# Performance work log

Hardware: AMD Instinct MI355X
Metric: run time of the kernel (lower is better)

Reference implementation:

```python
import jax, jax.numpy as jnp
import numpy as np

EPS = 1e-12

def _l2norm(x):
    # F.normalize(p=2, dim=1)
    n = jnp.sqrt(jnp.sum(x * x, axis=1, keepdims=True))
    return x / jnp.maximum(n, EPS)

def _sage(h, c, W, b):
    # Bundler: Linear(concat(h, mean_neigh)) -> l2 normalize -> relu
    z = jnp.concatenate([h, c], axis=1) @ W + b
    return jax.nn.relu(_l2norm(z))

def _block_diag(blocks):
    # blocks: [B, K, K] -> dense [B*K, B*K] block-diagonal (torch.block_diag of per-graph S^T A S)
    B, K, _ = blocks.shape
    out = jnp.zeros((B * K, B * K), blocks.dtype)
    base = (jnp.arange(B) * K)[:, None, None]
    r = base + jnp.arange(K)[None, :, None]
    c = base + jnp.arange(K)[None, None, :]
    return out.at[r, c].set(blocks)

def setup_inputs() -> dict:
    key = jax.random.key(0)
    k0, k1, k2, k3, k4 = jax.random.split(key, 5)
    B, n, F, K, E = 64, 1024, 128, 128, 16384
    N = B * n
    h = jax.random.normal(k0, (N, F), dtype=jnp.float32)
    src_local = jax.random.randint(k1, (B, E), 0, n, dtype=jnp.int32)
    dst_local = jax.random.randint(k2, (B, E), 0, n, dtype=jnp.int32)
    s = 1.0 / np.sqrt(2 * F)
    W_feat = jax.random.normal(k3, (2 * F, F), dtype=jnp.float32) * s
    b_feat = jnp.zeros((F,), dtype=jnp.float32)
    W_pool = jax.random.normal(k4, (2 * F, K), dtype=jnp.float32) * s
    b_pool = jnp.zeros((K,), dtype=jnp.float32)
    return {"h": h, "src_local": src_local, "dst_local": dst_local,
            "W_feat": W_feat, "b_feat": b_feat, "W_pool": W_pool, "b_pool": b_pool}

def reference(h, src_local, dst_local, W_feat, b_feat, W_pool, b_pool):
    N, F = h.shape
    B, E = src_local.shape
    n = N // B
    K = W_pool.shape[1]
    # per-graph local edge ids -> global ids (batched graph)
    off = (jnp.arange(B, dtype=src_local.dtype) * n)[:, None]
    src = (src_local + off).reshape(-1)  # [B*E]
    dst = (dst_local + off).reshape(-1)
    # MeanAggregator: c[i] = mean over in-neighbors (edges src->dst) of h[src]
    deg = jax.ops.segment_sum(jnp.ones((B * E,), h.dtype), dst, num_segments=N)
    c = jax.ops.segment_sum(h[src], dst, num_segments=N) / jnp.maximum(deg, 1.0)[:, None]
    feat = _sage(h, c, W_feat, b_feat)                     # [N, F]
    assign = jax.nn.softmax(_sage(h, c, W_pool, b_pool), axis=1)  # [N, K] per-graph soft assignment
    # adj_external(transpose=True): adj[u, v] = 1 for edge (u -> v)
    # AS[u] = sum over edges (u->v) of assign[v]
    AS = jax.ops.segment_sum(assign[dst], src, num_segments=N)    # [N, K]
    S_r = assign.reshape(B, n, K)
    AS_r = AS.reshape(B, n, K)
    feat_r = feat.reshape(B, n, F)
    # h_new = S^T feat (block-diagonal S => per-graph contraction)
    h_new = jnp.einsum('bnk,bnf->bkf', S_r, feat_r).reshape(B * K, F)
    # adj_new = S^T (adj S), block diagonal across graphs
    blocks = jnp.einsum('bnk,bnl->bkl', S_r, AS_r)
    adj_new = _block_diag(blocks)
    return adj_new, h_new
```

## Files before the change

### kernel.cpp

```cpp
#include <hip/hip_runtime.h>
#include <hip/hip_bf16.h>
#include <cstddef>

#define B_    64
#define NPG   1024
#define F_    128
#define K_    128
#define E_    16384
#define N_    (B_*NPG)
#define BE_   (B_*E_)
#define ADJ_DIM 8192
#define ADJ_ELEMS 67108864UL

typedef __bf16 bf16x8 __attribute__((ext_vector_type(8)));
typedef float  f32x4  __attribute__((ext_vector_type(4)));

__device__ inline float b2f(unsigned short u) {
  return __uint_as_float(((unsigned)u) << 16);
}
__device__ inline unsigned short f2b(float f) {
  __bf16 b = (__bf16)f;
  return *reinterpret_cast<unsigned short*>(&b);
}

__global__ void k_hbf(const float* __restrict__ h, unsigned short* __restrict__ hb) {
  int i = blockIdx.x * 256 + threadIdx.x;
  float4 v = reinterpret_cast<const float4*>(h)[i];
  ushort4 o;
  o.x = f2b(v.x); o.y = f2b(v.y); o.z = f2b(v.z); o.w = f2b(v.w);
  reinterpret_cast<ushort4*>(hb)[i] = o;
}

__global__ void k_count(const int* __restrict__ srcl, const int* __restrict__ dstl,
                        int* __restrict__ deg_in, int* __restrict__ deg_out) {
  int i = blockIdx.x * 256 + threadIdx.x;
  int b = i >> 14;
  int base = b << 10;
  atomicAdd(&deg_in[dstl[i] + base], 1);
  atomicAdd(&deg_out[srcl[i] + base], 1);
}

__global__ __launch_bounds__(1024) void k_scan(const int* __restrict__ deg,
                                               int* __restrict__ off, int* __restrict__ cur) {
  int b = blockIdx.x, t = threadIdx.x;
  int v = deg[b * NPG + t];
  int lane = t & 63, wid = t >> 6;
  int x = v;
  #pragma unroll
  for (int d = 1; d < 64; d <<= 1) {
    int y = __shfl_up(x, d, 64);
    if (lane >= d) x += y;
  }
  __shared__ int wsum[16];
  if (lane == 63) wsum[wid] = x;
  __syncthreads();
  if (t < 16) {
    int s = wsum[t];
    #pragma unroll
    for (int d = 1; d < 16; d <<= 1) {
      int y = __shfl_up(s, d, 16);
      if (t >= d) s += y;
    }
    wsum[t] = s;
  }
  __syncthreads();
  int woff = wid ? wsum[wid - 1] : 0;
  int o = b * E_ + woff + x - v;
  off[b * NPG + t] = o;
  cur[b * NPG + t] = o;
}

__global__ void k_build(const int* __restrict__ srcl, const int* __restrict__ dstl,
                        int* __restrict__ cur_in, int* __restrict__ cur_out,
                        int* __restrict__ ebd_src, int* __restrict__ ebs_dst) {
  int i = blockIdx.x * 256 + threadIdx.x;
  int b = i >> 14;
  int base = b << 10;
  int s = srcl[i] + base, d = dstl[i] + base;
  int p = atomicAdd(&cur_in[d], 1);
  ebd_src[p] = s;
  int q = atomicAdd(&cur_out[s], 1);
  ebs_dst[q] = d;
}

__global__ void k_gather_c(const unsigned short* __restrict__ hb, const int* __restrict__ elist,
                           const int* __restrict__ off, const int* __restrict__ deg,
                           unsigned short* __restrict__ cb, float* __restrict__ adj) {
  {
    float4 z4 = make_float4(0.f, 0.f, 0.f, 0.f);
    float4* dst = reinterpret_cast<float4*>(adj) + (size_t)blockIdx.x * 1024 + threadIdx.x;
    #pragma unroll
    for (int r = 0; r < 4; ++r) dst[r * 256] = z4;
  }
  int w = threadIdx.x >> 6, lane = threadIdx.x & 63;
  int node = blockIdx.x * 4 + w;
  int o = off[node], d = deg[node];
  float accx = 0.f, accy = 0.f;
  int e = o, end = o + d;
  while (e < end) {
    int cnt = end - e; if (cnt > 64) cnt = 64;
    int sidx = (lane < cnt) ? elist[e + lane] : 0;
    for (int j = 0; j < cnt; ++j) {
      int s = __shfl(sidx, j, 64);
      unsigned v = *reinterpret_cast<const unsigned*>(hb + (size_t)s * 128 + lane * 2);
      accx += __uint_as_float((v & 0xffffu) << 16);
      accy += __uint_as_float(v & 0xffff0000u);
    }
    e += cnt;
  }
  float inv = 1.0f / fmaxf((float)d, 1.0f);
  accx *= inv; accy *= inv;
  unsigned ov = (unsigned)f2b(accx) | ((unsigned)f2b(accy) << 16);
  *reinterpret_cast<unsigned*>(cb + (size_t)node * 128 + lane * 2) = ov;
}

__global__ void k_gather_as(const unsigned short* __restrict__ rows, const int* __restrict__ elist,
                            const int* __restrict__ off, const int* __restrict__ deg,
                            unsigned short* __restrict__ outb) {
  int w = threadIdx.x >> 6, lane = threadIdx.x & 63;
  int node = blockIdx.x * 4 + w;
  int o = off[node], d = deg[node];
  float accx = 0.f, accy = 0.f;
  int e = o, end = o + d;
  while (e < end) {
    int cnt = end - e; if (cnt > 64) cnt = 64;
    int sidx = (lane < cnt) ? elist[e + lane] : 0;
    for (int j = 0; j < cnt; ++j) {
      int s = __shfl(sidx, j, 64);
      unsigned v = *reinterpret_cast<const unsigned*>(rows + (size_t)s * 256 + lane * 2);
      accx += __uint_as_float((v & 0xffffu) << 16);
      accy += __uint_as_float(v & 0xffff0000u);
    }
    e += cnt;
  }
  unsigned ov = (unsigned)f2b(accx) | ((unsigned)f2b(accy) << 16);
  *reinterpret_cast<unsigned*>(outb + (size_t)node * 128 + lane * 2) = ov;
}

__global__ void k_wt(const float* __restrict__ Wf, const float* __restrict__ Wp,
                     __bf16* __restrict__ Wt) {
  int j = blockIdx.x;
  int k = threadIdx.x;
  const float* W = (j < 128) ? Wf : Wp;
  int jj = j & 127;
  Wt[j * 256 + k] = (__bf16)W[k * 128 + jj];
}

__global__ __launch_bounds__(512) void k_gemm(const __bf16* __restrict__ hb,
                                              const __bf16* __restrict__ cb,
                                              const __bf16* __restrict__ Wt,
                                              const float* __restrict__ bfeat,
                                              const float* __restrict__ bpool,
                                              __bf16* __restrict__ Z) {
  __shared__ char smem[69632];
  __bf16* A_lds = (__bf16*)smem;
  __bf16* B_lds = (__bf16*)(smem + 8192);
  const int t = threadIdx.x;
  const int wid = t >> 6, lane = t & 63;
  const int wm = wid >> 1, wn = wid & 1;
  const int lo = lane & 15, hi = lane >> 4;
  const int m0 = blockIdx.x * 128;

  float bias[8];
  const float* bsrc = wn ? bpool : bfeat;
  #pragma unroll
  for (int nf = 0; nf < 8; ++nf) bias[nf] = bsrc[nf * 16 + lo];

  f32x4 acc[2][8];
  #pragma unroll
  for (int mf = 0; mf < 2; ++mf)
    #pragma unroll
    for (int nf = 0; nf < 8; ++nf) acc[mf][nf] = (f32x4){0.f, 0.f, 0.f, 0.f};

  const int am = t >> 2, akq = (t & 3) * 8;
  const int bj = t >> 1, bh = (t & 1) * 16;

  for (int ks = 0; ks < 8; ++ks) {
    const int kb = ks * 32;
    const __bf16* __restrict__ X = (kb < 128) ? hb : cb;
    const int kbb = kb & 127;
    *reinterpret_cast<bf16x8*>(A_lds + am * 32 + akq) =
        *reinterpret_cast<const bf16x8*>(X + (size_t)(m0 + am) * 128 + kbb + akq);
    {
      bf16x8 b0 = *reinterpret_cast<const bf16x8*>(Wt + bj * 256 + kb + bh);
      bf16x8 b1 = *reinterpret_cast<const bf16x8*>(Wt + bj * 256 + kb + bh + 8);
      *reinterpret_cast<bf16x8*>(B_lds + bj * 40 + bh) = b0;
      *reinterpret_cast<bf16x8*>(B_lds + bj * 40 + bh + 8) = b1;
    }
    __syncthreads();
    bf16x8 a[2], b[8];
    #pragma unroll
    for (int mf = 0; mf < 2; ++mf)
      a[mf] = *reinterpret_cast<const bf16x8*>(A_lds + (wm * 32 + mf * 16 + lo) * 32 + hi * 8);
    #pragma unroll
    for (int nf = 0; nf < 8; ++nf)
      b[nf] = *reinterpret_cast<const bf16x8*>(B_lds + (wn * 128 + nf * 16 + lo) * 40 + hi * 8);
    #pragma unroll
    for (int mf = 0; mf < 2; ++mf)
      #pragma unroll
      for (int nf = 0; nf < 8; ++nf)
        acc[mf][nf] = __builtin_amdgcn_mfma_f32_16x16x32_bf16(a[mf], b[nf], acc[mf][nf], 0, 0, 0);
    __syncthreads();
  }

  __bf16* obuf = (__bf16*)(smem + wid * 8704);
  #pragma unroll
  for (int mf = 0; mf < 2; ++mf) {
    #pragma unroll
    for (int r = 0; r < 4; ++r) {
      float v[8];
      #pragma unroll
      for (int nf = 0; nf < 8; ++nf) v[nf] = acc[mf][nf][r] + bias[nf];
      float ss = 0.f;
      #pragma unroll
      for (int nf = 0; nf < 8; ++nf) ss += v[nf] * v[nf];
      ss += __shfl_xor(ss, 1, 64); ss += __shfl_xor(ss, 2, 64);
      ss += __shfl_xor(ss, 4, 64); ss += __shfl_xor(ss, 8, 64);
      float rn = 1.0f / fmaxf(sqrtf(ss), 1e-12f);
      #pragma unroll
      for (int nf = 0; nf < 8; ++nf) v[nf] = fmaxf(v[nf] * rn, 0.f);
      if (wn) {
        float mx = v[0];
        #pragma unroll
        for (int nf = 1; nf < 8; ++nf) mx = fmaxf(mx, v[nf]);
        mx = fmaxf(mx, __shfl_xor(mx, 1, 64)); mx = fmaxf(mx, __shfl_xor(mx, 2, 64));
        mx = fmaxf(mx, __shfl_xor(mx, 4, 64)); mx = fmaxf(mx, __shfl_xor(mx, 8, 64));
        float es = 0.f;
        #pragma unroll
        for (int nf = 0; nf < 8; ++nf) { v[nf] = __expf(v[nf] - mx); es += v[nf]; }
        es += __shfl_xor(es, 1, 64); es += __shfl_xor(es, 2, 64);
        es += __shfl_xor(es, 4, 64); es += __shfl_xor(es, 8, 64);
        float inv = 1.0f / es;
        #pragma unroll
        for (int nf = 0; nf < 8; ++nf) v[nf] *= inv;
      }
      int row = mf * 16 + hi * 4 + r;
      #pragma unroll
      for (int nf = 0; nf < 8; ++nf) obuf[row * 136 + nf * 16 + lo] = (__bf16)v[nf];
    }
  }
  __syncthreads();
  #pragma unroll
  for (int i = 0; i < 8; ++i) {
    int r = i * 4 + hi;
    bf16x8 d = *reinterpret_cast<const bf16x8*>(obuf + r * 136 + lo * 8);
    int node = m0 + wm * 32 + r;
    *reinterpret_cast<bf16x8*>(Z + (size_t)node * 256 + wn * 128 + lo * 8) = d;
  }
}

__global__ __launch_bounds__(256) void k_pool(const unsigned short* __restrict__ Zb,
                                              const unsigned short* __restrict__ ASb,
                                              float* __restrict__ part) {
  const int blk = blockIdx.x;
  const int b = blk >> 3, ch = (blk >> 2) & 1, q = blk & 3;
  const int n0 = b * NPG + q * 256;
  const unsigned short* __restrict__ Xbase = ch ? ASb : Zb;
  const int xstride = ch ? 128 : 256;
  __shared__ float Ss[16][128];
  __shared__ float Xs[16][128];
  const int t = threadIdx.x;
  const int tx = t & 15, ty = t >> 4;
  float acc[8][8];
  #pragma unroll
  for (int i = 0; i < 8; ++i)
    #pragma unroll
    for (int j = 0; j < 8; ++j) acc[i][j] = 0.f;

  for (int nc = 0; nc < 256; nc += 16) {
    #pragma unroll
    for (int r = 0; r < 2; ++r) {
      int idx = t * 2 + r;
      int nn = idx >> 5;
      int jq = (idx & 31) * 4;
      int n = n0 + nc + nn;
      ushort4 sv = *reinterpret_cast<const ushort4*>(Zb + (size_t)n * 256 + 128 + jq);
      *reinterpret_cast<float4*>(&Ss[nn][jq]) =
          make_float4(b2f(sv.x), b2f(sv.y), b2f(sv.z), b2f(sv.w));
      ushort4 xv = *reinterpret_cast<const ushort4*>(Xbase + (size_t)n * xstride + jq);
      *reinterpret_cast<float4*>(&Xs[nn][jq]) =
          make_float4(b2f(xv.x), b2f(xv.y), b2f(xv.z), b2f(xv.w));
    }
    __syncthreads();
    #pragma unroll
    for (int nn = 0; nn < 16; ++nn) {
      float a[8], x[8];
      #pragma unroll
      for (int i = 0; i < 8; ++i) a[i] = Ss[nn][ty * 8 + i];
      #pragma unroll
      for (int j = 0; j < 8; ++j) x[j] = Xs[nn][tx * 8 + j];
      #pragma unroll
      for (int i = 0; i < 8; ++i)
        #pragma unroll
        for (int j = 0; j < 8; ++j) acc[i][j] += a[i] * x[j];
    }
    __syncthreads();
  }
  float* dst = part + (size_t)blk * 16384;
  #pragma unroll
  for (int i = 0; i < 8; ++i) {
    *reinterpret_cast<float4*>(dst + (ty * 8 + i) * 128 + tx * 8) =
        make_float4(acc[i][0], acc[i][1], acc[i][2], acc[i][3]);
    *reinterpret_cast<float4*>(dst + (ty * 8 + i) * 128 + tx * 8 + 4) =
        make_float4(acc[i][4], acc[i][5], acc[i][6], acc[i][7]);
  }
}

__global__ void k_reduce(const float* __restrict__ part, float* __restrict__ h_new,
                         float* __restrict__ blocks) {
  int i = blockIdx.x * 256 + threadIdx.x;
  int bc = i >> 14;
  int r = i & 16383;
  int b = bc >> 1, ch = bc & 1;
  size_t base = ((size_t)(b * 8 + ch * 4)) * 16384 + r;
  float v = part[base] + part[base + 16384] + part[base + 32768] + part[base + 49152];
  if (ch == 0) h_new[(size_t)b * 16384 + r] = v;
  else blocks[(size_t)b * 16384 + r] = v;
}

__global__ void k_scatter(const float* __restrict__ blocks, float* __restrict__ adj) {
  int i = blockIdx.x * 256 + threadIdx.x;
  int b = i >> 14;
  int k = (i >> 7) & 127;
  int l = i & 127;
  adj[(size_t)(b * 128 + k) * ADJ_DIM + b * 128 + l] = blocks[i];
}

extern "C" void kernel_launch(void* const* d_in, const int* in_sizes, int n_in,
                              void* d_out, int out_size, void* d_ws, size_t ws_size,
                              hipStream_t stream) {
  (void)in_sizes; (void)n_in; (void)out_size; (void)ws_size;
  const float* h   = (const float*)d_in[0];
  const int* srcl  = (const int*)d_in[1];
  const int* dstl  = (const int*)d_in[2];
  const float* Wf  = (const float*)d_in[3];
  const float* bfe = (const float*)d_in[4];
  const float* Wp  = (const float*)d_in[5];
  const float* bpo = (const float*)d_in[6];

  float* out   = (float*)d_out;
  float* adj   = out;
  float* h_new = out + ADJ_ELEMS;

  char* W = (char*)d_ws;
  int* deg_in   = (int*)W;
  int* deg_out  = deg_in + N_;
  int* off_in   = deg_out + N_;
  int* cur_in   = off_in + N_;
  int* off_out  = cur_in + N_;
  int* cur_out  = off_out + N_;
  int* ebd_src  = cur_out + N_;
  int* ebs_dst  = ebd_src + BE_;
  unsigned short* hb  = (unsigned short*)(ebs_dst + BE_);
  unsigned short* cb  = hb + 8388608UL;
  unsigned short* Zb  = cb + 8388608UL;
  unsigned short* ASb = Zb + 16777216UL;
  __bf16* Wt          = (__bf16*)(ASb + 8388608UL);
  float* part         = (float*)((unsigned short*)Wt + 65536UL);
  float* blocks       = part + 8388608UL;

  hipMemsetAsync(deg_in, 0, 2UL * N_ * sizeof(int), stream);
  k_hbf<<<8192, 256, 0, stream>>>(h, hb);
  k_wt<<<256, 256, 0, stream>>>(Wf, Wp, Wt);
  k_count<<<BE_ / 256, 256, 0, stream>>>(srcl, dstl, deg_in, deg_out);
  k_scan<<<B_, 1024, 0, stream>>>(deg_in, off_in, cur_in);
  k_scan<<<B_, 1024, 0, stream>>>(deg_out, off_out, cur_out);
  k_build<<<BE_ / 256, 256, 0, stream>>>(srcl, dstl, cur_in, cur_out, ebd_src, ebs_dst);
  k_gather_c<<<N_ / 4, 256, 0, stream>>>(hb, ebd_src, off_in, deg_in, cb, adj);
  k_gemm<<<N_ / 128, 512, 0, stream>>>((const __bf16*)hb, (const __bf16*)cb, Wt, bfe, bpo, (__bf16*)Zb);
  k_gather_as<<<N_ / 4, 256, 0, stream>>>(Zb + 128, ebs_dst, off_out, deg_out, ASb);
  k_pool<<<512, 256, 0, stream>>>(Zb, ASb, part);
  k_reduce<<<8192, 256, 0, stream>>>(part, h_new, blocks);
  k_scatter<<<4096, 256, 0, stream>>>(blocks, adj);
}
```

Before: 654.2 us.

## Vectorize gathers, move pooling to MFMA and drop reduce/scatter via atomics

```diff
diff --git a/kernel.cpp b/kernel.cpp
--- a/kernel.cpp
+++ b/kernel.cpp
@@ -14,13 +14,24 @@
 
 typedef __bf16 bf16x8 __attribute__((ext_vector_type(8)));
 typedef float  f32x4  __attribute__((ext_vector_type(4)));
-
-__device__ inline float b2f(unsigned short u) {
-  return __uint_as_float(((unsigned)u) << 16);
-}
+typedef unsigned short u16x8 __attribute__((ext_vector_type(8)));
+
 __device__ inline unsigned short f2b(float f) {
   __bf16 b = (__bf16)f;
   return *reinterpret_cast<unsigned short*>(&b);
+}
+__device__ inline unsigned packbf(float x, float y) {
+  return (unsigned)f2b(x) | ((unsigned)f2b(y) << 16);
+}
+__device__ inline void addrow(float* a, uint4 v) {
+  a[0] += __uint_as_float(v.x << 16);
+  a[1] += __uint_as_float(v.x & 0xffff0000u);
+  a[2] += __uint_as_float(v.y << 16);
+  a[3] += __uint_as_float(v.y & 0xffff0000u);
+  a[4] += __uint_as_float(v.z << 16);
+  a[5] += __uint_as_float(v.z & 0xffff0000u);
+  a[6] += __uint_as_float(v.w << 16);
+  a[7] += __uint_as_float(v.w & 0xffff0000u);
 }
 
 __global__ void k_hbf(const float* __restrict__ h, unsigned short* __restrict__ hb) {
@@ -83,58 +94,52 @@
   ebs_dst[q] = d;
 }
 
-__global__ void k_gather_c(const unsigned short* __restrict__ hb, const int* __restrict__ elist,
-                           const int* __restrict__ off, const int* __restrict__ deg,
-                           unsigned short* __restrict__ cb, float* __restrict__ adj) {
-  {
+template<int ROWSTRIDE, bool MEAN, bool ZERO>
+__global__ void k_gather(const unsigned short* __restrict__ rows, const int* __restrict__ elist,
+                         const int* __restrict__ off, const int* __restrict__ deg,
+                         unsigned short* __restrict__ outb, float* __restrict__ adj) {
+  if (ZERO) {
     float4 z4 = make_float4(0.f, 0.f, 0.f, 0.f);
     float4* dst = reinterpret_cast<float4*>(adj) + (size_t)blockIdx.x * 1024 + threadIdx.x;
     #pragma unroll
     for (int r = 0; r < 4; ++r) dst[r * 256] = z4;
   }
   int w = threadIdx.x >> 6, lane = threadIdx.x & 63;
+  int g = lane >> 4, li = lane & 15;
   int node = blockIdx.x * 4 + w;
   int o = off[node], d = deg[node];
-  float accx = 0.f, accy = 0.f;
+  float acc[8];
+  #pragma unroll
+  for (int i = 0; i < 8; ++i) acc[i] = 0.f;
+  const unsigned short* rbase = rows + li * 8;
   int e = o, end = o + d;
   while (e < end) {
     int cnt = end - e; if (cnt > 64) cnt = 64;
     int sidx = (lane < cnt) ? elist[e + lane] : 0;
-    for (int j = 0; j < cnt; ++j) {
+    for (int t = 0; t * 4 < cnt; ++t) {
+      int j = t * 4 + g;
       int s = __shfl(sidx, j, 64);
-      unsigned v = *reinterpret_cast<const unsigned*>(hb + (size_t)s * 128 + lane * 2);
-      accx += __uint_as_float((v & 0xffffu) << 16);
-      accy += __uint_as_float(v & 0xffff0000u);
+      if (j < cnt) {
+        uint4 v = *reinterpret_cast<const uint4*>(rbase + (size_t)s * ROWSTRIDE);
+        addrow(acc, v);
+      }
     }
     e += cnt;
   }
-  float inv = 1.0f / fmaxf((float)d, 1.0f);
-  accx *= inv; accy *= inv;
-  unsigned ov = (unsigned)f2b(accx) | ((unsigned)f2b(accy) << 16);
-  *reinterpret_cast<unsigned*>(cb + (size_t)node * 128 + lane * 2) = ov;
-}
-
-__global__ void k_gather_as(const unsigned short* __restrict__ rows, const int* __restrict__ elist,
-                            const int* __restrict__ off, const int* __restrict__ deg,
-                            unsigned short* __restrict__ outb) {
-  int w = threadIdx.x >> 6, lane = threadIdx.x & 63;
-  int node = blockIdx.x * 4 + w;
-  int o = off[node], d = deg[node];
-  float accx = 0.f, accy = 0.f;
-  int e = o, end = o + d;
-  while (e < end) {
-    int cnt = end - e; if (cnt > 64) cnt = 64;
-    int sidx = (lane < cnt) ? elist[e + lane] : 0;
-    for (int j = 0; j < cnt; ++j) {
-      int s = __shfl(sidx, j, 64);
-      unsigned v = *reinterpret_cast<const unsigned*>(rows + (size_t)s * 256 + lane * 2);
-      accx += __uint_as_float((v & 0xffffu) << 16);
-      accy += __uint_as_float(v & 0xffff0000u);
-    }
-    e += cnt;
-  }
-  unsigned ov = (unsigned)f2b(accx) | ((unsigned)f2b(accy) << 16);
-  *reinterpret_cast<unsigned*>(outb + (size_t)node * 128 + lane * 2) = ov;
+  #pragma unroll
+  for (int i = 0; i < 8; ++i) {
+    acc[i] += __shfl_xor(acc[i], 16, 64);
+    acc[i] += __shfl_xor(acc[i], 32, 64);
+  }
+  if (g == 0) {
+    float sc = MEAN ? (1.0f / fmaxf((float)d, 1.0f)) : 1.0f;
+    uint4 ov;
+    ov.x = packbf(acc[0] * sc, acc[1] * sc);
+    ov.y = packbf(acc[2] * sc, acc[3] * sc);
+    ov.z = packbf(acc[4] * sc, acc[5] * sc);
+    ov.w = packbf(acc[6] * sc, acc[7] * sc);
+    *reinterpret_cast<uint4*>(outb + (size_t)node * 128 + li * 8) = ov;
+  }
 }
 
 __global__ void k_wt(const float* __restrict__ Wf, const float* __restrict__ Wp,
@@ -249,81 +254,86 @@
   }
 }
 
-__global__ __launch_bounds__(256) void k_pool(const unsigned short* __restrict__ Zb,
-                                              const unsigned short* __restrict__ ASb,
-                                              float* __restrict__ part) {
+__global__ __launch_bounds__(256) void k_poolm(const unsigned short* __restrict__ Zb,
+                                               const unsigned short* __restrict__ ASb,
+                                               float* __restrict__ h_new,
+                                               float* __restrict__ adj) {
   const int blk = blockIdx.x;
-  const int b = blk >> 3, ch = (blk >> 2) & 1, q = blk & 3;
-  const int n0 = b * NPG + q * 256;
-  const unsigned short* __restrict__ Xbase = ch ? ASb : Zb;
-  const int xstride = ch ? 128 : 256;
-  __shared__ float Ss[16][128];
-  __shared__ float Xs[16][128];
+  const int b = blk >> 2, ch = (blk >> 1) & 1, nh = blk & 1;
+  const int n0 = b * NPG + nh * 512;
+  __shared__ __align__(16) unsigned short ST[128 * 40];
+  __shared__ __align__(16) unsigned short XT[128 * 40];
   const int t = threadIdx.x;
-  const int tx = t & 15, ty = t >> 4;
-  float acc[8][8];
-  #pragma unroll
-  for (int i = 0; i < 8; ++i)
-    #pragma unroll
-    for (int j = 0; j < 8; ++j) acc[i][j] = 0.f;
-
-  for (int nc = 0; nc < 256; nc += 16) {
-    #pragma unroll
-    for (int r = 0; r < 2; ++r) {
-      int idx = t * 2 + r;
-      int nn = idx >> 5;
-      int jq = (idx & 31) * 4;
-      int n = n0 + nc + nn;
-      ushort4 sv = *reinterpret_cast<const ushort4*>(Zb + (size_t)n * 256 + 128 + jq);
-      *reinterpret_cast<float4*>(&Ss[nn][jq]) =
-          make_float4(b2f(sv.x), b2f(sv.y), b2f(sv.z), b2f(sv.w));
-      ushort4 xv = *reinterpret_cast<const ushort4*>(Xbase + (size_t)n * xstride + jq);
-      *reinterpret_cast<float4*>(&Xs[nn][jq]) =
-          make_float4(b2f(xv.x), b2f(xv.y), b2f(xv.z), b2f(xv.w));
+  const int wid = t >> 6, lane = t & 63;
+  const int lo = lane & 15, hi = lane >> 4;
+  const int wk = wid >> 1, wf = wid & 1;
+  const int sn = t & 31, sc0 = (t >> 5) * 16;
+
+  f32x4 acc[4][4];
+  #pragma unroll
+  for (int m = 0; m < 4; ++m)
+    #pragma unroll
+    for (int f = 0; f < 4; ++f) acc[m][f] = (f32x4){0.f, 0.f, 0.f, 0.f};
+
+  for (int nc = 0; nc < 512; nc += 32) {
+    int n = n0 + nc + sn;
+    {
+      u16x8 s0 = *reinterpret_cast<const u16x8*>(Zb + (size_t)n * 256 + 128 + sc0);
+      u16x8 s1 = *reinterpret_cast<const u16x8*>(Zb + (size_t)n * 256 + 128 + sc0 + 8);
+      #pragma unroll
+      for (int i = 0; i < 8; ++i) ST[(sc0 + i) * 40 + sn] = s0[i];
+      #pragma unroll
+      for (int i = 0; i < 8; ++i) ST[(sc0 + 8 + i) * 40 + sn] = s1[i];
+    }
+    {
+      const unsigned short* xr = ch ? (ASb + (size_t)n * 128 + sc0)
+                                    : (Zb + (size_t)n * 256 + sc0);
+      u16x8 x0 = *reinterpret_cast<const u16x8*>(xr);
+      u16x8 x1 = *reinterpret_cast<const u16x8*>(xr + 8);
+      #pragma unroll
+      for (int i = 0; i < 8; ++i) XT[(sc0 + i) * 40 + sn] = x0[i];
+      #pragma unroll
+      for (int i = 0; i < 8; ++i) XT[(sc0 + 8 + i) * 40 + sn] = x1[i];
     }
     __syncthreads();
-    #pragma unroll
-    for (int nn = 0; nn < 16; ++nn) {
-      float a[8], x[8];
-      #pragma unroll
-      for (int i = 0; i < 8; ++i) a[i] = Ss[nn][ty * 8 + i];
-      #pragma unroll
-      for (int j = 0; j < 8; ++j) x[j] = Xs[nn][tx * 8 + j];
-      #pragma unroll
-      for (int i = 0; i < 8; ++i)
-        #pragma unroll
-        for (int j = 0; j < 8; ++j) acc[i][j] += a[i] * x[j];
-    }
+    bf16x8 a[4], bb[4];
+    #pragma unroll
+    for (int m = 0; m < 4; ++m)
+      a[m] = *reinterpret_cast<const bf16x8*>(ST + (wk * 64 + m * 16 + lo) * 40 + hi * 8);
+    #pragma unroll
+    for (int f = 0; f < 4; ++f)
+      bb[f] = *reinterpret_cast<const bf16x8*>(XT + (wf * 64 + f * 16 + lo) * 40 + hi * 8);
+    #pragma unroll
+    for (int m = 0; m < 4; ++m)
+      #pragma unroll
+      for (int f = 0; f < 4; ++f)
+        acc[m][f] = __builtin_amdgcn_mfma_f32_16x16x32_bf16(a[m], bb[f], acc[m][f], 0, 0, 0);
     __syncthreads();
   }
-  float* dst = part + (size_t)blk * 16384;
-  #pragma unroll
-  for (int i = 0; i < 8; ++i) {
-    *reinterpret_cast<float4*>(dst + (ty * 8 + i) * 128 + tx * 8) =
-        make_float4(acc[i][0], acc[i][1], acc[i][2], acc[i][3]);
-    *reinterpret_cast<float4*>(dst + (ty * 8 + i) * 128 + tx * 8 + 4) =
-        make_float4(acc[i][4], acc[i][5], acc[i][6], acc[i][7]);
-  }
-}
-
-__global__ void k_reduce(const float* __restrict__ part, float* __restrict__ h_new,
-                         float* __restrict__ blocks) {
-  int i = blockIdx.x * 256 + threadIdx.x;
-  int bc = i >> 14;
-  int r = i & 16383;
-  int b = bc >> 1, ch = bc & 1;
-  size_t base = ((size_t)(b * 8 + ch * 4)) * 16384 + r;
-  float v = part[base] + part[base + 16384] + part[base + 32768] + part[base + 49152];
-  if (ch == 0) h_new[(size_t)b * 16384 + r] = v;
-  else blocks[(size_t)b * 16384 + r] = v;
-}
-
-__global__ void k_scatter(const float* __restrict__ blocks, float* __restrict__ adj) {
-  int i = blockIdx.x * 256 + threadIdx.x;
-  int b = i >> 14;
-  int k = (i >> 7) & 127;
-  int l = i & 127;
-  adj[(size_t)(b * 128 + k) * ADJ_DIM + b * 128 + l] = blocks[i];
+
+  if (ch == 0) {
+    #pragma unroll
+    for (int m = 0; m < 4; ++m)
+      #pragma unroll
+      for (int f = 0; f < 4; ++f)
+        #pragma unroll
+        for (int r = 0; r < 4; ++r) {
+          int k = wk * 64 + m * 16 + hi * 4 + r;
+          int fc = wf * 64 + f * 16 + lo;
+          atomicAdd(&h_new[(size_t)(b * 128 + k) * 128 + fc], acc[m][f][r]);
+        }
+  } else {
+    #pragma unroll
+    for (int m = 0; m < 4; ++m)
+      #pragma unroll
+      for (int f = 0; f < 4; ++f)
+        #pragma unroll
+        for (int r = 0; r < 4; ++r) {
+          int k = wk * 64 + m * 16 + hi * 4 + r;
+          int fc = wf * 64 + f * 16 + lo;
+          atomicAdd(&adj[(size_t)(b * 128 + k) * ADJ_DIM + b * 128 + fc], acc[m][f][r]);
+        }
+  }
 }
 
 extern "C" void kernel_launch(void* const* d_in, const int* in_sizes, int n_in,
@@ -356,20 +366,17 @@
   unsigned short* Zb  = cb + 8388608UL;
   unsigned short* ASb = Zb + 16777216UL;
   __bf16* Wt          = (__bf16*)(ASb + 8388608UL);
-  float* part         = (float*)((unsigned short*)Wt + 65536UL);
-  float* blocks       = part + 8388608UL;
 
   hipMemsetAsync(deg_in, 0, 2UL * N_ * sizeof(int), stream);
+  hipMemsetAsync(h_new, 0, (size_t)B_ * K_ * F_ * sizeof(float), stream);
   k_hbf<<<8192, 256, 0, stream>>>(h, hb);
   k_wt<<<256, 256, 0, stream>>>(Wf, Wp, Wt);
   k_count<<<BE_ / 256, 256, 0, stream>>>(srcl, dstl, deg_in, deg_out);
   k_scan<<<B_, 1024, 0, stream>>>(deg_in, off_in, cur_in);
   k_scan<<<B_, 1024, 0, stream>>>(deg_out, off_out, cur_out);
   k_build<<<BE_ / 256, 256, 0, stream>>>(srcl, dstl, cur_in, cur_out, ebd_src, ebs_dst);
-  k_gather_c<<<N_ / 4, 256, 0, stream>>>(hb, ebd_src, off_in, deg_in, cb, adj);
+  k_gather<128, true, true><<<N_ / 4, 256, 0, stream>>>(hb, ebd_src, off_in, deg_in, cb, adj);
   k_gemm<<<N_ / 128, 512, 0, stream>>>((const __bf16*)hb, (const __bf16*)cb, Wt, bfe, bpo, (__bf16*)Zb);
-  k_gather_as<<<N_ / 4, 256, 0, stream>>>(Zb + 128, ebs_dst, off_out, deg_out, ASb);
-  k_pool<<<512, 256, 0, stream>>>(Zb, ASb, part);
-  k_reduce<<<8192, 256, 0, stream>>>(part, h_new, blocks);
-  k_scatter<<<4096, 256, 0, stream>>>(blocks, adj);
-}
+  k_gather<256, false, false><<<N_ / 4, 256, 0, stream>>>(Zb + 128, ebs_dst, off_out, deg_out, ASb, nullptr);
+  k_poolm<<<256, 256, 0, stream>>>(Zb, ASb, h_new, adj);
+}
```

After: 570.1 us. 12.9% less time.
